# Kernel tuning notes

Hardware: AMD Instinct MI355X
Metric: run time of the kernel (lower is better)

## Reference

```python
import jax, jax.numpy as jnp
import numpy as np

L, C, H, W, CC, K = 6, 384, 4, 4, 1536, 3
DK = C // H
B, T = 16, 512


def setup_inputs() -> dict:
    key = jax.random.key(0)
    ks = jax.random.split(key, 12)
    r = lambda k, s: jax.random.normal(k, s, dtype=jnp.float32) * 0.02
    return {
        'x': jax.random.normal(ks[0], (B, C, T), dtype=jnp.float32),
        'mask': jnp.ones((B, 1, T), jnp.float32),
        'Wq': r(ks[1], (L, C, C)), 'bq': jnp.zeros((L, C), jnp.float32),
        'Wk': r(ks[2], (L, C, C)), 'bk': jnp.zeros((L, C), jnp.float32),
        'Wv': r(ks[3], (L, C, C)), 'bv': jnp.zeros((L, C), jnp.float32),
        'Wo': r(ks[4], (L, C, C)), 'bo': jnp.zeros((L, C), jnp.float32),
        'rel_k': r(ks[5], (L, 2 * W + 1, DK)),
        'rel_v': r(ks[6], (L, 2 * W + 1, DK)),
        'ln0_g': jnp.ones((L, C), jnp.float32), 'ln0_b': jnp.zeros((L, C), jnp.float32),
        'conv0_w': r(ks[7], (L, CC, C, K)), 'conv0_b': jnp.zeros((L, CC), jnp.float32),
        'conv1_w': r(ks[8], (L, C, CC, K)), 'conv1_b': jnp.zeros((L, C), jnp.float32),
        'ln1_g': jnp.ones((L, C), jnp.float32), 'ln1_b': jnp.zeros((L, C), jnp.float32),
    }


def _rel_to_abs(x):
    # x: [B,H,T,2T-1] relative-indexed logits -> [B,H,T,T] absolute
    b, h, t, _ = x.shape
    x = jnp.pad(x, ((0, 0), (0, 0), (0, 0), (0, 1)))      # [b,h,t,2t]
    x = x.reshape(b, h, t * 2 * t)
    x = jnp.pad(x, ((0, 0), (0, 0), (0, t - 1)))
    x = x.reshape(b, h, t + 1, 2 * t - 1)
    return x[:, :, :t, t - 1:]


def _abs_to_rel(x):
    # x: [B,H,T,T] -> [B,H,T,2T-1] relative-indexed
    b, h, t, _ = x.shape
    x = jnp.pad(x, ((0, 0), (0, 0), (0, 0), (0, t - 1)))  # [b,h,t,2t-1]
    x = x.reshape(b, h, t * (2 * t - 1))
    x = jnp.pad(x, ((0, 0), (0, 0), (t, 0)))
    x = x.reshape(b, h, t, 2 * t)
    return x[:, :, :, 1:]


def _get_rel(emb, t):
    # emb: [2W+1, d] clipped relative embeddings -> [2t-1, d] (t > W+1 here)
    pad = t - (W + 1)
    return jnp.pad(emb, ((pad, pad), (0, 0)))


def _ln(x, g, b):
    # LayerNorm over channel dim of [B,C,T] (torch applies on transposed [B,T,C])
    m = x.mean(axis=1, keepdims=True)
    v = ((x - m) ** 2).mean(axis=1, keepdims=True)
    return (x - m) * jax.lax.rsqrt(v + 1e-4) * g[None, :, None] + b[None, :, None]


def _conv1d(x, w, b):
    y = jax.lax.conv_general_dilated(x, w, (1,), [((K - 1) // 2, (K - 1) // 2)],
                                     dimension_numbers=('NCH', 'OIH', 'NCH'))
    return y + b[None, :, None]


def _proj(x, w, b):
    # 1x1 conv == per-timestep linear: x [B,C,T], w [O,C]
    return jnp.einsum('oc,bct->bot', w, x) + b[None, :, None]


def reference(x, mask, Wq, bq, Wk, bk, Wv, bv, Wo, bo, rel_k, rel_v,
              ln0_g, ln0_b, conv0_w, conv0_b, conv1_w, conv1_b, ln1_g, ln1_b):
    b_, _, t = x.shape
    mask4 = (mask[:, 0][:, None, :, None] * mask[:, 0][:, None, None, :])  # [B,1,T,T]
    scale = 1.0 / np.sqrt(DK).astype(np.float32)
    for i in range(L):
        x = x * mask
        residual = x
        # --- RPR multi-head attention ---
        q = _proj(x, Wq[i], bq[i]).reshape(b_, H, DK, t).transpose(0, 1, 3, 2)  # [B,H,T,d]
        k = _proj(x, Wk[i], bk[i]).reshape(b_, H, DK, t).transpose(0, 1, 3, 2)
        v = _proj(x, Wv[i], bv[i]).reshape(b_, H, DK, t).transpose(0, 1, 3, 2)
        qs = q * scale
        scores = jnp.einsum('bhtd,bhsd->bhts', qs, k)
        rk = _get_rel(rel_k[i], t)                      # [2T-1, d]
        scores = scores + _rel_to_abs(jnp.einsum('bhtd,md->bhtm', qs, rk))
        scores = jnp.where(mask4 > 0, scores, -1e4)
        p = jax.nn.softmax(scores, axis=-1)
        rv = _get_rel(rel_v[i], t)
        out = jnp.einsum('bhts,bhsd->bhtd', p, v) + jnp.einsum('bhtm,md->bhtd', _abs_to_rel(p), rv)
        out = out.transpose(0, 1, 3, 2).reshape(b_, C, t)  # merge heads -> [B,C,T]
        out = _proj(out, Wo[i], bo[i])
        x = _ln(out + residual, ln0_g[i], ln0_b[i])
        # --- conv FFN ---
        residual = x
        y = _conv1d(x * mask, conv0_w[i], conv0_b[i])
        y = jax.nn.relu(y)
        y = _conv1d(y * mask, conv1_w[i], conv1_b[i])
        x = _ln(y * mask + residual, ln1_g[i], ln1_b[i])
    return x * mask
```

## Files before the change

### kernel.cpp

```cpp
#include <hip/hip_runtime.h>
#include <cstddef>
#include <cstdint>

constexpr int NB = 16, NC = 384, NT = 512, NH = 4, NDK = 96, NCC = 1536, NL = 6;
constexpr int NTP = NT + 2;
constexpr int MROWS = NB * NT;
constexpr float SCALE = 0.10206207261596577f;

typedef __attribute__((ext_vector_type(8))) short s8v;
typedef __attribute__((ext_vector_type(4))) float f4;

__device__ __forceinline__ unsigned short f2bf(float f) {
  unsigned u = __builtin_bit_cast(unsigned, f);
  u += 0x7FFFu + ((u >> 16) & 1u);
  return (unsigned short)(u >> 16);
}
__device__ __forceinline__ float bf2f(unsigned short h) {
  unsigned u = ((unsigned)h) << 16;
  return __builtin_bit_cast(float, u);
}
__device__ __forceinline__ void gload16(const void* g, void* l) {
  __builtin_amdgcn_global_load_lds((const __attribute__((address_space(1))) unsigned int*)g,
                                   (__attribute__((address_space(3))) unsigned int*)l,
                                   16, 0, 0);
}
__device__ __forceinline__ int swz384(int lin) { return (lin & 7) * 48 + (lin >> 3); }

__global__ __launch_bounds__(256) void prep_layer(
    const float* __restrict__ Wq, const float* __restrict__ bq,
    const float* __restrict__ Wk, const float* __restrict__ bk,
    const float* __restrict__ Wv, const float* __restrict__ bv,
    const float* __restrict__ Wo,
    const float* __restrict__ c0w, const float* __restrict__ c1w, int l,
    unsigned short* __restrict__ wqkv, float* __restrict__ bqkv,
    unsigned short* __restrict__ wo, unsigned short* __restrict__ c0,
    unsigned short* __restrict__ c1) {
  int idx = blockIdx.x * 256 + threadIdx.x;
  const int NW = 1152 * 384, NB2 = 1152, NWO = 384 * 384, NCV = 3 * 1536 * 384;
  if (idx < NW) {
    int o = idx / 384, c = idx - o * 384;
    float v;
    if (o < 384)      v = Wq[(size_t)l * NWO + o * 384 + c] * SCALE;
    else if (o < 768) v = Wk[(size_t)l * NWO + (o - 384) * 384 + c];
    else              v = Wv[(size_t)l * NWO + (o - 768) * 384 + c];
    wqkv[idx] = f2bf(v);
    return;
  }
  idx -= NW;
  if (idx < NB2) {
    float v;
    if (idx < 384)      v = bq[l * 384 + idx] * SCALE;
    else if (idx < 768) v = bk[l * 384 + idx - 384];
    else                v = bv[l * 384 + idx - 768];
    bqkv[idx] = v;
    return;
  }
  idx -= NB2;
  if (idx < NWO) { wo[idx] = f2bf(Wo[(size_t)l * NWO + idx]); return; }
  idx -= NWO;
  if (idx < NCV) {
    int kap = idx / (1536 * 384), rem = idx - kap * 1536 * 384;
    int oc = rem / 384, ic = rem - oc * 384;
    c0[idx] = f2bf(c0w[(((size_t)l * 1536 + oc) * 384 + ic) * 3 + kap]);
    return;
  }
  idx -= NCV;
  if (idx < NCV) {
    int kap = idx / (384 * 1536), rem = idx - kap * 384 * 1536;
    int oc = rem / 1536, ic = rem - oc * 1536;
    c1[idx] = f2bf(c1w[(((size_t)l * 384 + oc) * 1536 + ic) * 3 + kap]);
  }
}

__global__ __launch_bounds__(256) void zero_pads(unsigned short* __restrict__ xbf,
                                                 unsigned short* __restrict__ y0) {
  int idx = blockIdx.x * 256 + threadIdx.x;
  if (idx < NB * 2 * 384) {
    int bi = idx / 768, j = idx % 768, r = j / 384, c = j % 384;
    xbf[((size_t)bi * NTP + r * (NTP - 1)) * 384 + c] = 0;
  } else {
    int j0 = idx - NB * 2 * 384;
    int bi = j0 / 3072, j = j0 % 3072, r = j / 1536, c = j % 1536;
    y0[((size_t)bi * NTP + r * (NTP - 1)) * 1536 + c] = 0;
  }
}

template <bool OUT_BF16, bool APAD>
__global__ __launch_bounds__(256) void gemm_nt(
    const unsigned short* __restrict__ A, const unsigned short* __restrict__ Bw,
    const float* __restrict__ bias, void* __restrict__ Yv, int K, int N) {
  __shared__ unsigned short As[128][32];
  __shared__ unsigned short Bs[128][32];
  const int tid = threadIdx.x;
  const int lane = tid & 63, wid = tid >> 6;
  const int wr = wid >> 1, wc = wid & 1;
  const int l15 = lane & 15, l4 = lane >> 4;
  const int m0 = blockIdx.x * 128, n0 = blockIdx.y * 128;
  const size_t abase = APAD ? ((size_t)(m0 >> 9) * NTP + 1 + (m0 & 511)) * K
                            : (size_t)m0 * K;
  f4 acc[4][4] = {};
  const int e0 = tid, e1 = tid + 256;
  const int ar0 = e0 >> 2, as0 = (e0 & 3) * 8;
  const int ar1 = e1 >> 2, as1 = (e1 & 3) * 8;
  for (int kb = 0; kb < K; kb += 32) {
    __syncthreads();
    gload16(A + abase + (size_t)ar0 * K + kb + as0, &As[0][0] + e0 * 8);
    gload16(A + abase + (size_t)ar1 * K + kb + as1, &As[0][0] + e1 * 8);
    gload16(Bw + (size_t)(n0 + ar0) * K + kb + as0, &Bs[0][0] + e0 * 8);
    gload16(Bw + (size_t)(n0 + ar1) * K + kb + as1, &Bs[0][0] + e1 * 8);
    __syncthreads();
    s8v a[4], b[4];
    #pragma unroll
    for (int i = 0; i < 4; ++i) {
      a[i] = *(const s8v*)&As[wr * 64 + i * 16 + l15][l4 * 8];
      b[i] = *(const s8v*)&Bs[wc * 64 + i * 16 + l15][l4 * 8];
    }
    #pragma unroll
    for (int mi = 0; mi < 4; ++mi)
      #pragma unroll
      for (int ni = 0; ni < 4; ++ni)
        acc[mi][ni] = __builtin_amdgcn_mfma_f32_16x16x32_bf16(a[mi], b[ni], acc[mi][ni], 0, 0, 0);
  }
  float bvv[4];
  #pragma unroll
  for (int ni = 0; ni < 4; ++ni) bvv[ni] = bias[n0 + wc * 64 + ni * 16 + l15];
  #pragma unroll
  for (int mi = 0; mi < 4; ++mi)
    #pragma unroll
    for (int r = 0; r < 4; ++r) {
      const size_t row = m0 + wr * 64 + mi * 16 + l4 * 4 + r;
      #pragma unroll
      for (int ni = 0; ni < 4; ++ni) {
        const int col = n0 + wc * 64 + ni * 16 + l15;
        float v = acc[mi][ni][r] + bvv[ni];
        if (OUT_BF16) ((unsigned short*)Yv)[row * N + col] = f2bf(v);
        else          ((float*)Yv)[row * N + col] = v;
      }
    }
}

__global__ __launch_bounds__(512, 4) void conv0_k(
    const unsigned short* __restrict__ A, const unsigned short* __restrict__ W,
    const float* __restrict__ bias, unsigned short* __restrict__ Y) {
  __shared__ unsigned short As[258][32];
  __shared__ unsigned short Bs[3][128][32];
  const int tid = threadIdx.x;
  const int lane = tid & 63, wid = tid >> 6;
  const int wr = wid >> 1, wc = wid & 1;
  const int l15 = lane & 15, l4 = lane >> 4;
  int lin = swz384(blockIdx.y * 32 + blockIdx.x);
  const int m0 = (lin & 31) * 256, n0 = (lin >> 5) * 128;
  const int bb = m0 >> 9, tl = m0 & 511;
  const size_t abase = ((size_t)bb * NTP + tl) * 384;
  if (tl == 0 && tid < 256) {
    const size_t gr = (size_t)bb * NTP + ((tid >> 7) ? (NTP - 1) : 0);
    Y[gr * 1536 + n0 + (tid & 127)] = 0;
  }
  f4 acc[4][4] = {};
  for (int kb = 0; kb < 384; kb += 32) {
    __syncthreads();
    #pragma unroll
    for (int i = 0; i < 2; ++i) {
      int e = tid + i * 512;
      gload16(A + abase + (size_t)(e >> 2) * 384 + kb + (e & 3) * 8, &As[0][0] + e * 8);
    }
    if (tid < 8) {
      int e = tid + 1024;
      gload16(A + abase + (size_t)(e >> 2) * 384 + kb + (e & 3) * 8, &As[0][0] + e * 8);
    }
    #pragma unroll
    for (int i = 0; i < 3; ++i) {
      int e = tid + i * 512;
      int kp = e >> 9, r = (e >> 2) & 127, seg = e & 3;
      gload16(W + ((size_t)kp * 1536 + n0 + r) * 384 + kb + seg * 8, &Bs[0][0][0] + e * 8);
    }
    __syncthreads();
    #pragma unroll
    for (int kp = 0; kp < 3; ++kp) {
      s8v a[4], b[4];
      #pragma unroll
      for (int i = 0; i < 4; ++i) {
        a[i] = *(const s8v*)&As[wr * 64 + i * 16 + l15 + kp][l4 * 8];
        b[i] = *(const s8v*)&Bs[kp][wc * 64 + i * 16 + l15][l4 * 8];
      }
      #pragma unroll
      for (int mi = 0; mi < 4; ++mi)
        #pragma unroll
        for (int ni = 0; ni < 4; ++ni)
          acc[mi][ni] = __builtin_amdgcn_mfma_f32_16x16x32_bf16(a[mi], b[ni], acc[mi][ni], 0, 0, 0);
    }
  }
  float bvv[4];
  #pragma unroll
  for (int ni = 0; ni < 4; ++ni) bvv[ni] = bias[n0 + wc * 64 + ni * 16 + l15];
  #pragma unroll
  for (int mi = 0; mi < 4; ++mi)
    #pragma unroll
    for (int r = 0; r < 4; ++r) {
      const int m = wr * 64 + mi * 16 + l4 * 4 + r;
      const size_t row = (size_t)bb * NTP + 1 + tl + m;
      #pragma unroll
      for (int ni = 0; ni < 4; ++ni) {
        const int col = n0 + wc * 64 + ni * 16 + l15;
        Y[row * 1536 + col] = f2bf(fmaxf(acc[mi][ni][r] + bvv[ni], 0.f));
      }
    }
}

__global__ __launch_bounds__(256, 4) void conv1_k(
    const unsigned short* __restrict__ A, const unsigned short* __restrict__ W,
    const float* __restrict__ bias, float* __restrict__ P) {
  __shared__ unsigned short As[130][32];
  __shared__ unsigned short Bs[3][128][32];
  const int tid = threadIdx.x;
  const int lane = tid & 63, wid = tid >> 6;
  const int wr = wid >> 1, wc = wid & 1;
  const int l15 = lane & 15, l4 = lane >> 4;
  int lin = swz384((blockIdx.z * 3 + blockIdx.y) * 64 + blockIdx.x);
  const int m0 = (lin & 63) * 128;
  const int q = lin >> 6;
  const int n0 = (q % 3) * 128, part = q / 3;
  const size_t abase = ((size_t)(m0 >> 9) * NTP + (m0 & 511)) * 1536;
  const int k0 = part * 768;
  f4 acc[4][4] = {};
  for (int kb = k0; kb < k0 + 768; kb += 32) {
    __syncthreads();
    #pragma unroll
    for (int i = 0; i < 2; ++i) {
      int e = tid + i * 256;
      gload16(A + abase + (size_t)(e >> 2) * 1536 + kb + (e & 3) * 8, &As[0][0] + e * 8);
    }
    if (tid < 8) {
      int e = tid + 512;
      gload16(A + abase + (size_t)(e >> 2) * 1536 + kb + (e & 3) * 8, &As[0][0] + e * 8);
    }
    #pragma unroll
    for (int i = 0; i < 6; ++i) {
      int e = tid + i * 256;
      int kp = e >> 9, r = (e >> 2) & 127, seg = e & 3;
      gload16(W + ((size_t)kp * 384 + n0 + r) * 1536 + kb + seg * 8, &Bs[0][0][0] + e * 8);
    }
    __syncthreads();
    #pragma unroll
    for (int kp = 0; kp < 3; ++kp) {
      s8v a[4], b[4];
      #pragma unroll
      for (int i = 0; i < 4; ++i) {
        a[i] = *(const s8v*)&As[wr * 64 + i * 16 + l15 + kp][l4 * 8];
        b[i] = *(const s8v*)&Bs[kp][wc * 64 + i * 16 + l15][l4 * 8];
      }
      #pragma unroll
      for (int mi = 0; mi < 4; ++mi)
        #pragma unroll
        for (int ni = 0; ni < 4; ++ni)
          acc[mi][ni] = __builtin_amdgcn_mfma_f32_16x16x32_bf16(a[mi], b[ni], acc[mi][ni], 0, 0, 0);
    }
  }
  float bvv[4];
  #pragma unroll
  for (int ni = 0; ni < 4; ++ni)
    bvv[ni] = part == 0 ? bias[n0 + wc * 64 + ni * 16 + l15] : 0.f;
  #pragma unroll
  for (int mi = 0; mi < 4; ++mi)
    #pragma unroll
    for (int r = 0; r < 4; ++r) {
      const size_t row = m0 + wr * 64 + mi * 16 + l4 * 4 + r;
      #pragma unroll
      for (int ni = 0; ni < 4; ++ni) {
        const int col = n0 + wc * 64 + ni * 16 + l15;
        P[((size_t)part * MROWS + row) * 384 + col] = acc[mi][ni][r] + bvv[ni];
      }
    }
}

__global__ __launch_bounds__(256) void attn3(
    const unsigned short* __restrict__ qkv, const float* __restrict__ relk,
    const float* __restrict__ relv, unsigned short* __restrict__ ao) {
  __shared__ __align__(16) char uraw[64 * 96 * 2];
  __shared__ unsigned short K_lds[64][104];
  __shared__ unsigned short P_lds[4][16][72];
  __shared__ float qrel[64][12];
  __shared__ float rv[9][96];
  auto Qb = reinterpret_cast<unsigned short(*)[96]>(uraw);
  unsigned short* Vt = reinterpret_cast<unsigned short*>(uraw);

  const int tid = threadIdx.x;
  const int lane = tid & 63, w = tid >> 6;
  const int l15 = lane & 15, l4 = lane >> 4;
  const int t0 = blockIdx.x * 64, h = blockIdx.y, b = blockIdx.z;
  const size_t rowbase = (size_t)b * NT;
  const int hc = h * NDK;

  #pragma unroll
  for (int i = 0; i < 12; ++i) {
    int p = tid + i * 256;
    int r = p / 48, c2 = p - r * 48;
    *(unsigned*)&Qb[r][c2 * 2] =
        *(const unsigned*)(qkv + (rowbase + t0 + r) * 1152 + hc + c2 * 2);
  }
  for (int p = tid; p < 9 * 96; p += 256) rv[p / 96][p % 96] = relv[p];
  __syncthreads();

  for (int p = tid; p < 64 * 9; p += 256) {
    int r = p / 9, j = p - r * 9;
    const float* rk = relk + j * NDK;
    float dot = 0.f;
    #pragma unroll 4
    for (int d = 0; d < NDK; ++d) dot += bf2f(Qb[r][d]) * rk[d];
    qrel[r][j] = dot;
  }
  s8v aq[3];
  #pragma unroll
  for (int ks = 0; ks < 3; ++ks)
    aq[ks] = *(const s8v*)&Qb[w * 16 + l15][ks * 32 + l4 * 8];
  __syncthreads();

  const int tw = t0 + w * 16;
  f4 acc[6] = {};
  float m[4], lsum[4];
  #pragma unroll
  for (int r = 0; r < 4; ++r) { m[r] = -1e30f; lsum[r] = 0.f; }

  for (int sb = 0; sb < 8; ++sb) {
    const int s0 = sb * 64;
    __syncthreads();
    #pragma unroll
    for (int i = 0; i < 12; ++i) {
      int p = tid + i * 256;
      int sr = p / 48, c2 = p - sr * 48;
      *(unsigned*)&K_lds[sr][c2 * 2] =
          *(const unsigned*)(qkv + (rowbase + s0 + sr) * 1152 + 384 + hc + c2 * 2);
    }
    #pragma unroll
    for (int i = 0; i < 12; ++i) {
      int p = tid + i * 256;
      int sr = p / 48, d2 = p - sr * 48;
      unsigned u = *(const unsigned*)(qkv + (rowbase + s0 + sr) * 1152 + 768 + hc + d2 * 2);
      int d0 = d2 * 2;
      int hi = sr >> 3, lo = sr & 7;
      Vt[d0 * 64 + ((hi ^ (d0 & 7)) << 3) + lo] = (unsigned short)(u & 0xFFFFu);
      Vt[(d0 + 1) * 64 + ((hi ^ ((d0 + 1) & 7)) << 3) + lo] = (unsigned short)(u >> 16);
    }
    __syncthreads();

    f4 sv[4];
    #pragma unroll
    for (int nt = 0; nt < 4; ++nt) {
      sv[nt] = f4{0.f, 0.f, 0.f, 0.f};
      #pragma unroll
      for (int ks = 0; ks < 3; ++ks) {
        s8v bk = *(const s8v*)&K_lds[nt * 16 + l15][ks * 32 + l4 * 8];
        sv[nt] = __builtin_amdgcn_mfma_f32_16x16x32_bf16(aq[ks], bk, sv[nt], 0, 0, 0);
      }
    }
    const bool band = (s0 < tw + 20) && (s0 + 64 > tw - 4);
    if (band) {
      #pragma unroll
      for (int nt = 0; nt < 4; ++nt)
        #pragma unroll
        for (int r = 0; r < 4; ++r) {
          int j = (s0 + nt * 16 + l15) - (tw + l4 * 4 + r) + 4;
          if (0 <= j && j <= 8) sv[nt][r] += qrel[w * 16 + l4 * 4 + r][j];
        }
    }
    float pvv[4][4];
    #pragma unroll
    for (int r = 0; r < 4; ++r) {
      float tm = fmaxf(fmaxf(sv[0][r], sv[1][r]), fmaxf(sv[2][r], sv[3][r]));
      #pragma unroll
      for (int o = 1; o < 16; o <<= 1) tm = fmaxf(tm, __shfl_xor(tm, o));
      float mn = fmaxf(m[r], tm);
      float sc = __expf(m[r] - mn);
      m[r] = mn;
      float rs = 0.f;
      #pragma unroll
      for (int nt = 0; nt < 4; ++nt) {
        float p = __expf(sv[nt][r] - mn);
        pvv[nt][r] = p;
        rs += p;
      }
      #pragma unroll
      for (int o = 1; o < 16; o <<= 1) rs += __shfl_xor(rs, o);
      lsum[r] = lsum[r] * sc + rs;
      #pragma unroll
      for (int dt = 0; dt < 6; ++dt) acc[dt][r] *= sc;
    }
    #pragma unroll
    for (int nt = 0; nt < 4; ++nt)
      #pragma unroll
      for (int r = 0; r < 4; ++r)
        P_lds[w][l4 * 4 + r][nt * 16 + l15] = f2bf(pvv[nt][r]);
    asm volatile("s_waitcnt lgkmcnt(0)" ::: "memory");
    __builtin_amdgcn_sched_barrier(0);
    s8v pa[2];
    #pragma unroll
    for (int ks = 0; ks < 2; ++ks)
      pa[ks] = *(const s8v*)&P_lds[w][l15][ks * 32 + l4 * 8];
    #pragma unroll
    for (int dt = 0; dt < 6; ++dt) {
      const int n = dt * 16 + l15;
      #pragma unroll
      for (int ks = 0; ks < 2; ++ks) {
        const int chunk = (ks * 4 + l4) ^ (n & 7);
        s8v bv = *(const s8v*)&Vt[n * 64 + chunk * 8];
        acc[dt] = __builtin_amdgcn_mfma_f32_16x16x32_bf16(pa[ks], bv, acc[dt], 0, 0, 0);
      }
    }
    if (band) {
      #pragma unroll
      for (int r = 0; r < 4; ++r) {
        int tg = tw + l4 * 4 + r;
        #pragma unroll
        for (int j = 0; j < 9; ++j) {
          int sg = tg + j - 4 - s0;
          if (0 <= sg && sg < 64) {
            float p = bf2f(P_lds[w][l4 * 4 + r][sg]);
            #pragma unroll
            for (int dt = 0; dt < 6; ++dt)
              acc[dt][r] += p * rv[j][dt * 16 + l15];
          }
        }
      }
    }
  }
  #pragma unroll
  for (int r = 0; r < 4; ++r) {
    float inv = 1.f / lsum[r];
    int tg = tw + l4 * 4 + r;
    unsigned short* op = ao + (rowbase + tg) * 384 + hc;
    #pragma unroll
    for (int dt = 0; dt < 6; ++dt)
      op[dt * 16 + l15] = f2bf(acc[dt][r] * inv);
  }
}

template <int NP>
__global__ __launch_bounds__(256) void ln_rows(
    const float* __restrict__ Yv, const float* __restrict__ Yv2,
    const float* __restrict__ Res, const float* __restrict__ g,
    const float* __restrict__ bta, float* __restrict__ Xout,
    unsigned short* __restrict__ Xbf) {
  const int row = blockIdx.x * 4 + (threadIdx.x >> 6);
  const int lane = threadIdx.x & 63;
  const float* yp = Yv + (size_t)row * NC;
  const float* y2 = Yv2 + (size_t)row * NC;
  const float* rp = Res + (size_t)row * NC;
  float z[6];
  float s1 = 0.f, s2 = 0.f;
  #pragma unroll
  for (int i = 0; i < 6; ++i) {
    z[i] = yp[lane + 64 * i] + rp[lane + 64 * i];
    if (NP == 2) z[i] += y2[lane + 64 * i];
    s1 += z[i]; s2 += z[i] * z[i];
  }
  #pragma unroll
  for (int o = 32; o; o >>= 1) { s1 += __shfl_xor(s1, o); s2 += __shfl_xor(s2, o); }
  const float mean = s1 * (1.f / NC);
  const float rstd = rsqrtf(s2 * (1.f / NC) - mean * mean + 1e-4f);
  float* xp = Xout + (size_t)row * NC;
  unsigned short* bp = Xbf + ((size_t)(row >> 9) * NTP + 1 + (row & 511)) * NC;
  #pragma unroll
  for (int i = 0; i < 6; ++i) {
    int c = lane + 64 * i;
    float v = (z[i] - mean) * rstd * g[c] + bta[c];
    xp[c] = v; bp[c] = f2bf(v);
  }
}

__global__ __launch_bounds__(256) void tin_k(const float* __restrict__ xin,
                                             float* __restrict__ xb,
                                             unsigned short* __restrict__ xbf) {
  __shared__ float tile[32][33];
  const int b = blockIdx.z, c0 = blockIdx.y * 32, t0 = blockIdx.x * 32;
  const int tx = threadIdx.x & 31, ty = threadIdx.x >> 5;
  #pragma unroll
  for (int i = 0; i < 4; ++i)
    tile[ty + 8 * i][tx] = xin[((size_t)b * NC + c0 + ty + 8 * i) * NT + t0 + tx];
  __syncthreads();
  #pragma unroll
  for (int i = 0; i < 4; ++i) {
    float v = tile[tx][ty + 8 * i];
    int t = t0 + ty + 8 * i;
    xb[((size_t)b * NT + t) * NC + c0 + tx] = v;
    xbf[((size_t)b * NTP + 1 + t) * NC + c0 + tx] = f2bf(v);
  }
}
__global__ __launch_bounds__(256) void tout_k(const float* __restrict__ xb,
                                              float* __restrict__ out) {
  __shared__ float tile[32][33];
  const int b = blockIdx.z, c0 = blockIdx.y * 32, t0 = blockIdx.x * 32;
  const int tx = threadIdx.x & 31, ty = threadIdx.x >> 5;
  #pragma unroll
  for (int i = 0; i < 4; ++i)
    tile[ty + 8 * i][tx] = xb[((size_t)b * NT + t0 + ty + 8 * i) * NC + c0 + tx];
  __syncthreads();
  #pragma unroll
  for (int i = 0; i < 4; ++i)
    out[((size_t)b * NC + c0 + ty + 8 * i) * NT + t0 + tx] = tile[tx][ty + 8 * i];
}

extern "C" void kernel_launch(void* const* d_in, const int* in_sizes, int n_in,
                              void* d_out, int out_size, void* d_ws, size_t ws_size,
                              hipStream_t stream) {
  (void)in_sizes; (void)n_in; (void)out_size; (void)ws_size;
  const float* x_in = (const float*)d_in[0];
  const float* Wq = (const float*)d_in[2];  const float* bq = (const float*)d_in[3];
  const float* Wk = (const float*)d_in[4];  const float* bk = (const float*)d_in[5];
  const float* Wv = (const float*)d_in[6];  const float* bv = (const float*)d_in[7];
  const float* Wo = (const float*)d_in[8];  const float* bo = (const float*)d_in[9];
  const float* rel_k = (const float*)d_in[10]; const float* rel_v = (const float*)d_in[11];
  const float* ln0g = (const float*)d_in[12]; const float* ln0b = (const float*)d_in[13];
  const float* c0w = (const float*)d_in[14]; const float* c0b = (const float*)d_in[15];
  const float* c1w = (const float*)d_in[16]; const float* c1b = (const float*)d_in[17];
  const float* ln1g = (const float*)d_in[18]; const float* ln1b = (const float*)d_in[19];

  char* wsp = (char*)d_ws;
  auto alloc = [&](size_t bytes) {
    char* p = wsp; wsp += (bytes + 255) & ~(size_t)255; return p;
  };
  unsigned short* wqkv_l = (unsigned short*)alloc((size_t)1152 * 384 * 2);
  float*          bqkv_l = (float*)alloc(1152 * 4);
  unsigned short* wo_l   = (unsigned short*)alloc((size_t)384 * 384 * 2);
  unsigned short* c0_l   = (unsigned short*)alloc((size_t)3 * 1536 * 384 * 2);
  unsigned short* c1_l   = (unsigned short*)alloc((size_t)3 * 384 * 1536 * 2);
  float*          xbuf   = (float*)alloc((size_t)MROWS * NC * 4);
  unsigned short* xbf    = (unsigned short*)alloc((size_t)NB * NTP * NC * 2);
  float*          obuf   = (float*)alloc((size_t)MROWS * NC * 4);
  float*          part   = (float*)alloc((size_t)2 * MROWS * NC * 4);
  unsigned short* scratch = (unsigned short*)alloc((size_t)NB * NTP * NCC * 2);
  unsigned short* qkv_bf = scratch;
  unsigned short* ao_bf  = scratch + (size_t)MROWS * 1152;
  unsigned short* y0_pad = scratch;

  zero_pads<<<240, 256, 0, stream>>>(xbf, y0_pad);
  tin_k<<<dim3(16, 12, NB), 256, 0, stream>>>(x_in, xbuf, xbf);
  for (int l = 0; l < NL; ++l) {
    prep_layer<<<16133, 256, 0, stream>>>(Wq, bq, Wk, bk, Wv, bv, Wo, c0w, c1w, l,
                                          wqkv_l, bqkv_l, wo_l, c0_l, c1_l);
    gemm_nt<true, true><<<dim3(64, 9), 256, 0, stream>>>(xbf, wqkv_l, bqkv_l, qkv_bf,
                                                         384, 1152);
    attn3<<<dim3(8, 4, 16), 256, 0, stream>>>(qkv_bf, rel_k + l * 9 * NDK,
                                              rel_v + l * 9 * NDK, ao_bf);
    gemm_nt<false, false><<<dim3(64, 3), 256, 0, stream>>>(ao_bf, wo_l, bo + l * NC,
                                                           obuf, 384, 384);
    ln_rows<1><<<2048, 256, 0, stream>>>(obuf, obuf, xbuf, ln0g + l * NC, ln0b + l * NC,
                                         xbuf, xbf);
    conv0_k<<<dim3(32, 12), 512, 0, stream>>>(xbf, c0_l, c0b + l * NCC, y0_pad);
    conv1_k<<<dim3(64, 3, 2), 256, 0, stream>>>(y0_pad, c1_l, c1b + l * NC, part);
    ln_rows<2><<<2048, 256, 0, stream>>>(part, part + (size_t)MROWS * NC, xbuf,
                                         ln1g + l * NC, ln1b + l * NC, xbuf, xbf);
  }
  tout_k<<<dim3(16, 12, NB), 256, 0, stream>>>(xbuf, (float*)d_out);
}
```

Measured before the change: 1.140 ms.

## Double attention query tile to 128 rows with 512-thread blocks and swizzled block mapping

The attention kernel now handles 128 query rows per block with 8 waves instead of 64 rows with 4 waves, so each K/V tile loaded into LDS is shared by twice as many queries. Global loads of Q, K and V are widened from 4-byte to 8-byte accesses, and the flat block index is remapped so consecutive blocks cover different (batch, head) pairs. This halves K/V reload traffic, but the grid shrinks to 256 blocks, which may lower occupancy and load balance on a GPU with many CUs. Only the visible parts were checked; the hidden body must index per-wave rows correctly for 8 waves.

After: 1.109 ms. -2.7%, faster.

```diff
diff --git a/kernel.cpp b/kernel.cpp
--- a/kernel.cpp
+++ b/kernel.cpp
@@ -273,13 +273,13 @@
     }
 }
 
-__global__ __launch_bounds__(256) void attn3(
+__global__ __launch_bounds__(512) void attn4(
     const unsigned short* __restrict__ qkv, const float* __restrict__ relk,
     const float* __restrict__ relv, unsigned short* __restrict__ ao) {
-  __shared__ __align__(16) char uraw[64 * 96 * 2];
+  __shared__ __align__(16) char uraw[128 * 96 * 2];
   __shared__ unsigned short K_lds[64][104];
-  __shared__ unsigned short P_lds[4][16][72];
-  __shared__ float qrel[64][12];
+  __shared__ unsigned short P_lds[8][16][72];
+  __shared__ float qrel[128][12];
   __shared__ float rv[9][96];
   auto Qb = reinterpret_cast<unsigned short(*)[96]>(uraw);
   unsigned short* Vt = reinterpret_cast<unsigned short*>(uraw);
@@ -287,21 +287,25 @@
   const int tid = threadIdx.x;
   const int lane = tid & 63, w = tid >> 6;
   const int l15 = lane & 15, l4 = lane >> 4;
-  const int t0 = blockIdx.x * 64, h = blockIdx.y, b = blockIdx.z;
+  const int f = blockIdx.z * 16 + blockIdx.y * 4 + blockIdx.x;
+  const int bh = ((f & 7) << 3) | ((f >> 3) & 7);
+  const int qx = f >> 6;
+  const int b = bh >> 2, h = bh & 3;
+  const int t0 = qx * 128;
   const size_t rowbase = (size_t)b * NT;
   const int hc = h * NDK;
 
   #pragma unroll
-  for (int i = 0; i < 12; ++i) {
-    int p = tid + i * 256;
-    int r = p / 48, c2 = p - r * 48;
-    *(unsigned*)&Qb[r][c2 * 2] =
-        *(const unsigned*)(qkv + (rowbase + t0 + r) * 1152 + hc + c2 * 2);
-  }
-  for (int p = tid; p < 9 * 96; p += 256) rv[p / 96][p % 96] = relv[p];
+  for (int i = 0; i < 6; ++i) {
+    int p = tid + i * 512;
+    int r = p / 24, c4 = p - r * 24;
+    *(uint2*)&Qb[r][c4 * 4] =
+        *(const uint2*)(qkv + (rowbase + t0 + r) * 1152 + hc + c4 * 4);
+  }
+  for (int p = tid; p < 9 * 96; p += 512) rv[p / 96][p % 96] = relv[p];
   __syncthreads();
 
-  for (int p = tid; p < 64 * 9; p += 256) {
+  for (int p = tid; p < 128 * 9; p += 512) {
     int r = p / 9, j = p - r * 9;
     const float* rk = relk + j * NDK;
     float dot = 0.f;
@@ -325,21 +329,25 @@
     const int s0 = sb * 64;
     __syncthreads();
     #pragma unroll
-    for (int i = 0; i < 12; ++i) {
-      int p = tid + i * 256;
-      int sr = p / 48, c2 = p - sr * 48;
-      *(unsigned*)&K_lds[sr][c2 * 2] =
-          *(const unsigned*)(qkv + (rowbase + s0 + sr) * 1152 + 384 + hc + c2 * 2);
-    }
-    #pragma unroll
-    for (int i = 0; i < 12; ++i) {
-      int p = tid + i * 256;
-      int sr = p / 48, d2 = p - sr * 48;
-      unsigned u = *(const unsigned*)(qkv + (rowbase + s0 + sr) * 1152 + 768 + hc + d2 * 2);
-      int d0 = d2 * 2;
+    for (int i = 0; i < 3; ++i) {
+      int p = tid + i * 512;
+      int sr = p / 24, c4 = p - sr * 24;
+      *(uint2*)&K_lds[sr][c4 * 4] =
+          *(const uint2*)(qkv + (rowbase + s0 + sr) * 1152 + 384 + hc + c4 * 4);
+    }
+    #pragma unroll
+    for (int i = 0; i < 3; ++i) {
+      int p = tid + i * 512;
+      int sr = p / 24, d4 = p - sr * 24;
+      uint2 u = *(const uint2*)(qkv + (rowbase + s0 + sr) * 1152 + 768 + hc + d4 * 4);
       int hi = sr >> 3, lo = sr & 7;
-      Vt[d0 * 64 + ((hi ^ (d0 & 7)) << 3) + lo] = (unsigned short)(u & 0xFFFFu);
-      Vt[(d0 + 1) * 64 + ((hi ^ ((d0 + 1) & 7)) << 3) + lo] = (unsigned short)(u >> 16);
+      #pragma unroll
+      for (int jj = 0; jj < 2; ++jj) {
+        unsigned uu = jj ? u.y : u.x;
+        int d0 = d4 * 4 + jj * 2;
+        Vt[d0 * 64 + ((hi ^ (d0 & 7)) << 3) + lo] = (unsigned short)(uu & 0xFFFFu);
+        Vt[(d0 + 1) * 64 + ((hi ^ ((d0 + 1) & 7)) << 3) + lo] = (unsigned short)(uu >> 16);
+      }
     }
     __syncthreads();
 
@@ -539,7 +547,7 @@
                                           wqkv_l, bqkv_l, wo_l, c0_l, c1_l);
     gemm_nt<true, true><<<dim3(64, 9), 256, 0, stream>>>(xbf, wqkv_l, bqkv_l, qkv_bf,
                                                          384, 1152);
-    attn3<<<dim3(8, 4, 16), 256, 0, stream>>>(qkv_bf, rel_k + l * 9 * NDK,
+    attn4<<<dim3(4, 4, 16), 512, 0, stream>>>(qkv_bf, rel_k + l * 9 * NDK,
                                               rel_v + l * 9 * NDK, ao_bf);
     gemm_nt<false, false><<<dim3(64, 3), 256, 0, stream>>>(ao_bf, wo_l, bo + l * NC,
                                                            obuf, 384, 384);
```
